# Optimization experiments

Hardware: AMD Instinct MI355X
Metric: run time of the kernel (lower is better)

Reference implementation:

```python
import jax, jax.numpy as jnp
import numpy as np

B, NQ, NKV, D = 2, 2048, 2048, 1024
N_HEADS = 16
D_H = D // N_HEADS


def setup_inputs() -> dict:
    key = jax.random.key(0)
    ks = jax.random.split(key, 10)
    s = 0.02  # weight init scale
    return {
        "q": jax.random.normal(ks[0], (B, NQ, D), jnp.float32),
        "kv": jax.random.normal(ks[1], (B, NKV, D), jnp.float32),
        "Wq": jax.random.normal(ks[2], (D, D), jnp.float32) * s,
        "bq": jnp.zeros((D,), jnp.float32),
        "Wk": jax.random.normal(ks[3], (D, D), jnp.float32) * s,
        "bk": jnp.zeros((D,), jnp.float32),
        "Wv": jax.random.normal(ks[4], (D, D), jnp.float32) * s,
        "bv": jnp.zeros((D,), jnp.float32),
        "Wo": jax.random.normal(ks[5], (D, D), jnp.float32) * s,
        "bo": jnp.zeros((D,), jnp.float32),
    }


def reference(q, kv, Wq, bq, Wk, bk, Wv, bv, Wo, bo):
    # Linear projections (torch Linear: x @ W.T + b)
    qh = q @ Wq.T + bq   # [B, NQ, D]
    kh = kv @ Wk.T + bk  # [B, NKV, D]
    vh = kv @ Wv.T + bv  # [B, NKV, D]
    # Split heads: [B, N, H, d_h]
    qh = qh.reshape(B, NQ, N_HEADS, D_H)
    kh = kh.reshape(B, NKV, N_HEADS, D_H)
    vh = vh.reshape(B, NKV, N_HEADS, D_H)
    scale = 1.0 / jnp.sqrt(jnp.asarray(D_H, qh.dtype))
    # QK^T per head: [B, H, NQ, NKV]
    scores = jnp.einsum("bqhd,bkhd->bhqk", qh, kh) * scale
    att = jax.nn.softmax(scores, axis=-1)
    # dropout p=0.0 -> identity
    out = jnp.einsum("bhqk,bkhd->bqhd", att, vh)  # [B, NQ, H, d_h]
    out = out.reshape(B, NQ, D)
    return out @ Wo.T + bo
```

## Files before the change

kernel.cpp:

```cpp
#include <hip/hip_runtime.h>
#include <cstddef>
#include <cstdint>

using half4v  = __attribute__((ext_vector_type(4))) _Float16;
using half8   = __attribute__((ext_vector_type(8))) _Float16;
using floatx4 = __attribute__((ext_vector_type(4))) float;

#define B_   2
#define NQ_  2048
#define DM   1024
#define NH_  16
#define DH_  64
#define NTILES 32

__device__ __forceinline__ void async16(const _Float16* g, _Float16* l) {
    __builtin_amdgcn_global_load_lds(
        (const __attribute__((address_space(1))) unsigned int*)g,
        (__attribute__((address_space(3))) unsigned int*)l, 16, 0, 0);
}

__global__ __launch_bounds__(256) void cvt_all(
        const float* __restrict__ q,  const float* __restrict__ kv,
        const float* __restrict__ wq, const float* __restrict__ wk,
        const float* __restrict__ wv, const float* __restrict__ wo,
        _Float16* __restrict__ dq,  _Float16* __restrict__ dkv,
        _Float16* __restrict__ dwq, _Float16* __restrict__ dwk,
        _Float16* __restrict__ dwv, _Float16* __restrict__ dwo) {
    int blk = blockIdx.x;
    const float* s;
    _Float16* d;
    int base;
    if (blk < 2048)      { s = q;  d = dq;  base = blk; }
    else if (blk < 4096) { s = kv; d = dkv; base = blk - 2048; }
    else if (blk < 4608) { s = wq; d = dwq; base = blk - 4096; }
    else if (blk < 5120) { s = wk; d = dwk; base = blk - 4608; }
    else if (blk < 5632) { s = wv; d = dwv; base = blk - 5120; }
    else                 { s = wo; d = dwo; base = blk - 5632; }
    int i = base * 256 + threadIdx.x;
    const float4* s4 = (const float4*)s;
    float4 a = s4[2 * i], b = s4[2 * i + 1];
    half8 h;
    h[0] = (_Float16)a.x; h[1] = (_Float16)a.y; h[2] = (_Float16)a.z; h[3] = (_Float16)a.w;
    h[4] = (_Float16)b.x; h[5] = (_Float16)b.y; h[6] = (_Float16)b.z; h[7] = (_Float16)b.w;
    ((half8*)d)[i] = h;
}

__global__ __launch_bounds__(256, 3) void proj_qkv(
        const _Float16* __restrict__ q16, const _Float16* __restrict__ kv16,
        const _Float16* __restrict__ wqp, const _Float16* __restrict__ wkp,
        const _Float16* __restrict__ wvp,
        const float* __restrict__ bqp, const float* __restrict__ bkp,
        const float* __restrict__ bvp,
        _Float16* __restrict__ qh, _Float16* __restrict__ kh,
        _Float16* __restrict__ vt) {
    __shared__ _Float16 As[128 * 64];
    __shared__ _Float16 Bs[128 * 64];

    const int which = blockIdx.x >> 8;
    const int sub = blockIdx.x & 255;
    const _Float16* A = (which == 0) ? q16 : kv16;
    const _Float16* W = (which == 0) ? wqp : (which == 1) ? wkp : wvp;
    const float* bias = (which == 0) ? bqp : (which == 1) ? bkp : bvp;

    const int t = threadIdx.x;
    const int w = t >> 6, lane = t & 63;
    const int r16 = lane & 15, quad = lane >> 4;
    const int bm = (sub & 7) * 4 + ((sub >> 3) & 3);
    const int bn = sub >> 5;
    const int m0 = bm * 128, n0 = bn * 128;
    const int wm = w >> 1, wn = w & 1;

    floatx4 acc[4][4];
#pragma unroll
    for (int i = 0; i < 4; i++)
#pragma unroll
        for (int j = 0; j < 4; j++)
#pragma unroll
            for (int r = 0; r < 4; r++) acc[i][j][r] = 0.f;

    const int ph0 = quad ^ (r16 & 7), ph1 = ph0 ^ 4;

    for (int k0 = 0; k0 < DM; k0 += 64) {
        __syncthreads();
#pragma unroll
        for (int i = 0; i < 4; i++) {
            int P = i * 256 + t;
            int m = P >> 3, c = (P & 7) ^ (m & 7);
            async16(A + (size_t)(m0 + m) * DM + k0 + c * 8, &As[P * 8]);
            async16(W + (size_t)(n0 + m) * DM + k0 + c * 8, &Bs[P * 8]);
        }
        asm volatile("s_waitcnt vmcnt(0)" ::: "memory");
        __syncthreads();

        half8 af[4][2], bf[4][2];
#pragma unroll
        for (int mi = 0; mi < 4; mi++) {
            int m = wm * 64 + mi * 16 + r16;
            af[mi][0] = ((const half8*)As)[m * 8 + ph0];
            af[mi][1] = ((const half8*)As)[m * 8 + ph1];
        }
#pragma unroll
        for (int ni = 0; ni < 4; ni++) {
            int n = wn * 64 + ni * 16 + r16;
            bf[ni][0] = ((const half8*)Bs)[n * 8 + ph0];
            bf[ni][1] = ((const half8*)Bs)[n * 8 + ph1];
        }
#pragma unroll
        for (int kd = 0; kd < 2; kd++)
#pragma unroll
            for (int mi = 0; mi < 4; mi++)
#pragma unroll
                for (int ni = 0; ni < 4; ni++)
                    acc[mi][ni] = __builtin_amdgcn_mfma_f32_16x16x32_f16(
                        af[mi][kd], bf[ni][kd], acc[mi][ni], 0, 0, 0);
    }

    if (which < 2) {
        _Float16* C = (which == 0) ? qh : kh;
        const float esc = (which == 0) ? 0.125f : 1.0f;
#pragma unroll
        for (int mi = 0; mi < 4; mi++)
#pragma unroll
            for (int r = 0; r < 4; r++) {
                int row = m0 + wm * 64 + mi * 16 + quad * 4 + r;
#pragma unroll
                for (int ni = 0; ni < 4; ni++) {
                    int col = n0 + wn * 64 + ni * 16 + r16;
                    C[(size_t)row * DM + col] = (_Float16)((acc[mi][ni][r] + bias[col]) * esc);
                }
            }
    } else {
#pragma unroll
        for (int mi = 0; mi < 4; mi++) {
            int krow = m0 + wm * 64 + mi * 16 + quad * 4;
            int bb = krow >> 11, kk = krow & 2047;
#pragma unroll
            for (int ni = 0; ni < 4; ni++) {
                int col = n0 + wn * 64 + ni * 16 + r16;
                int hh = col >> 6, dd = col & 63;
                float bv = bias[col];
                half4v pk;
#pragma unroll
                for (int r = 0; r < 4; r++) pk[r] = (_Float16)(acc[mi][ni][r] + bv);
                *(half4v*)&vt[((size_t)((bb * NH_ + hh) * DH_ + dd)) * NQ_ + kk] = pk;
            }
        }
    }
}

__global__ __launch_bounds__(256, 4) void attn_mfma(const _Float16* __restrict__ Qg,
                                                    const _Float16* __restrict__ Kg,
                                                    const _Float16* __restrict__ Vt,
                                                    _Float16* __restrict__ Og) {
    __shared__ _Float16 Ps[64 * 64];
    __shared__ _Float16 Ks[2][64 * 64];
    __shared__ _Float16 Vs[2][64 * 64];

    const int t = threadIdx.x, w = t >> 6, lane = t & 63;
    const int r16 = lane & 15, quad = lane >> 4;
    const int blk = blockIdx.x;
    const int bh = (blk & 7) * 4 + ((blk >> 3) & 3);
    const int qt = blk >> 5;
    const int b = bh >> 4, h = bh & 15;

    const _Float16* qbase = Qg + (size_t)(b * NQ_ + qt * 64) * DM + h * DH_;
    const _Float16* kbase = Kg + (size_t)(b * NQ_) * DM + h * DH_;
    const _Float16* vbase = Vt + (size_t)bh * DH_ * NQ_;

#pragma unroll
    for (int i = 0; i < 2; i++) {
        int P = i * 256 + t;
        int m = P >> 3, c = (P & 7) ^ (m & 7);
        async16(qbase + (size_t)m * DM + c * 8, &Ps[P * 8]);
        async16(kbase + (size_t)m * DM + c * 8, &Ks[0][P * 8]);
        async16(vbase + (size_t)m * NQ_ + c * 8, &Vs[0][P * 8]);
    }
    asm volatile("s_waitcnt vmcnt(0)" ::: "memory");
    __syncthreads();

    const int ph0 = quad ^ (r16 & 7), ph1 = ph0 ^ 4;
    half8 Qf[2];
    {
        int m = w * 16 + r16;
        Qf[0] = ((const half8*)Ps)[m * 8 + ph0];
        Qf[1] = ((const half8*)Ps)[m * 8 + ph1];
    }

    floatx4 oaccT[4];
    float lacc = 0.f;
#pragma unroll
    for (int nd = 0; nd < 4; nd++)
#pragma unroll
        for (int r = 0; r < 4; r++) oaccT[nd][r] = 0.f;

    for (int kt = 0; kt < NTILES; kt++) {
        const int cur = kt & 1;
        asm volatile("s_waitcnt vmcnt(0)" ::: "memory");
        __syncthreads();

        if (kt + 1 < NTILES) {
            const int nxt = cur ^ 1;
#pragma unroll
            for (int i = 0; i < 2; i++) {
                int P = i * 256 + t;
                int m = P >> 3, c = (P & 7) ^ (m & 7);
                async16(kbase + (size_t)((kt + 1) * 64 + m) * DM + c * 8, &Ks[nxt][P * 8]);
                async16(vbase + (size_t)m * NQ_ + (kt + 1) * 64 + c * 8, &Vs[nxt][P * 8]);
            }
        }

        floatx4 sacc[4];
#pragma unroll
        for (int nk = 0; nk < 4; nk++)
#pragma unroll
            for (int r = 0; r < 4; r++) sacc[nk][r] = 0.f;
#pragma unroll
        for (int kd = 0; kd < 2; kd++)
#pragma unroll
            for (int nk = 0; nk < 4; nk++) {
                half8 kf = ((const half8*)Ks[cur])[(nk * 16 + r16) * 8 + (kd ? ph1 : ph0)];
                sacc[nk] = __builtin_amdgcn_mfma_f32_16x16x32_f16(kf, Qf[kd], sacc[nk], 0, 0, 0);
            }

        const int q = w * 16 + r16;
#pragma unroll
        for (int nk = 0; nk < 4; nk++) {
            float p0 = __expf(sacc[nk][0]);
            float p1 = __expf(sacc[nk][1]);
            float p2 = __expf(sacc[nk][2]);
            float p3 = __expf(sacc[nk][3]);
            lacc += (p0 + p1) + (p2 + p3);
            half4v pk;
            pk[0] = (_Float16)p0; pk[1] = (_Float16)p1;
            pk[2] = (_Float16)p2; pk[3] = (_Float16)p3;
            int phys = (nk * 2 + (quad >> 1)) ^ (r16 & 7);
            *(half4v*)&Ps[q * 64 + phys * 8 + (quad & 1) * 4] = pk;
        }

#pragma unroll
        for (int ks = 0; ks < 2; ks++) {
            half8 pf = ((const half8*)Ps)[q * 8 + ((ks * 4 + quad) ^ (r16 & 7))];
#pragma unroll
            for (int nd = 0; nd < 4; nd++) {
                half8 vf = ((const half8*)Vs[cur])[(nd * 16 + r16) * 8 + ((ks * 4 + quad) ^ (r16 & 7))];
                oaccT[nd] = __builtin_amdgcn_mfma_f32_16x16x32_f16(vf, pf, oaccT[nd], 0, 0, 0);
            }
        }
    }

    {
        float l = lacc;
        l += __shfl_xor(l, 16);
        l += __shfl_xor(l, 32);
        float inv = 1.f / l;
        int qrow = b * NQ_ + qt * 64 + w * 16 + r16;
#pragma unroll
        for (int nd = 0; nd < 4; nd++) {
            half4v o;
#pragma unroll
            for (int r = 0; r < 4; r++) o[r] = (_Float16)(oaccT[nd][r] * inv);
            *(half4v*)&Og[(size_t)qrow * DM + h * DH_ + nd * 16 + quad * 4] = o;
        }
    }
}

__global__ __launch_bounds__(256, 4) void gemm_o(const _Float16* __restrict__ A,
                                                 const _Float16* __restrict__ W,
                                                 const float* __restrict__ bias,
                                                 float* __restrict__ C) {
    __shared__ _Float16 As[64 * 64];
    __shared__ _Float16 Bs[64 * 64];

    const int t = threadIdx.x;
    const int w = t >> 6, lane = t & 63;
    const int r16 = lane & 15, quad = lane >> 4;
    const int blk = blockIdx.x;
    const int bm = (blk & 7) * 8 + ((blk >> 3) & 7);
    const int bn = blk >> 6;
    const int m0 = bm * 64, n0 = bn * 64;
    const int wm = w >> 1, wn = w & 1;

    floatx4 acc[2][2];
#pragma unroll
    for (int i = 0; i < 2; i++)
#pragma unroll
        for (int j = 0; j < 2; j++)
#pragma unroll
            for (int r = 0; r < 4; r++) acc[i][j][r] = 0.f;

    const int ph0 = quad ^ (r16 & 7), ph1 = ph0 ^ 4;

    for (int k0 = 0; k0 < DM; k0 += 64) {
        __syncthreads();
#pragma unroll
        for (int i = 0; i < 2; i++) {
            int P = i * 256 + t;
            int m = P >> 3, c = (P & 7) ^ (m & 7);
            async16(A + (size_t)(m0 + m) * DM + k0 + c * 8, &As[P * 8]);
            async16(W + (size_t)(n0 + m) * DM + k0 + c * 8, &Bs[P * 8]);
        }
        asm volatile("s_waitcnt vmcnt(0)" ::: "memory");
        __syncthreads();

        half8 af[2][2], bf[2][2];
#pragma unroll
        for (int mi = 0; mi < 2; mi++) {
            int m = wm * 32 + mi * 16 + r16;
            af[mi][0] = ((const half8*)As)[m * 8 + ph0];
            af[mi][1] = ((const half8*)As)[m * 8 + ph1];
        }
#pragma unroll
        for (int ni = 0; ni < 2; ni++) {
            int n = wn * 32 + ni * 16 + r16;
            bf[ni][0] = ((const half8*)Bs)[n * 8 + ph0];
            bf[ni][1] = ((const half8*)Bs)[n * 8 + ph1];
        }
#pragma unroll
        for (int kd = 0; kd < 2; kd++)
#pragma unroll
            for (int mi = 0; mi < 2; mi++)
#pragma unroll
                for (int ni = 0; ni < 2; ni++)
                    acc[mi][ni] = __builtin_amdgcn_mfma_f32_16x16x32_f16(
                        af[mi][kd], bf[ni][kd], acc[mi][ni], 0, 0, 0);
    }

#pragma unroll
    for (int mi = 0; mi < 2; mi++)
#pragma unroll
        for (int r = 0; r < 4; r++) {
            int row = m0 + wm * 32 + mi * 16 + quad * 4 + r;
#pragma unroll
            for (int ni = 0; ni < 2; ni++) {
                int col = n0 + wn * 32 + ni * 16 + r16;
                C[(size_t)row * DM + col] = acc[mi][ni][r] + bias[col];
            }
        }
}

extern "C" void kernel_launch(void* const* d_in, const int* in_sizes, int n_in,
                              void* d_out, int out_size, void* d_ws, size_t ws_size,
                              hipStream_t stream) {
    const float* q  = (const float*)d_in[0];
    const float* kv = (const float*)d_in[1];
    const float* Wq = (const float*)d_in[2];
    const float* bq = (const float*)d_in[3];
    const float* Wk = (const float*)d_in[4];
    const float* bk = (const float*)d_in[5];
    const float* Wv = (const float*)d_in[6];
    const float* bv = (const float*)d_in[7];
    const float* Wo = (const float*)d_in[8];
    const float* bo = (const float*)d_in[9];

    char* ws = (char*)d_ws;
    _Float16* q16  = (_Float16*)(ws);
    _Float16* kv16 = (_Float16*)(ws + (size_t)(8  << 20));
    _Float16* w16q = (_Float16*)(ws + (size_t)(16 << 20));
    _Float16* w16k = (_Float16*)(ws + (size_t)(18 << 20));
    _Float16* w16v = (_Float16*)(ws + (size_t)(20 << 20));
    _Float16* w16o = (_Float16*)(ws + (size_t)(22 << 20));
    _Float16* qh16 = (_Float16*)(ws + (size_t)(24 << 20));
    _Float16* kh16 = (_Float16*)(ws + (size_t)(32 << 20));
    _Float16* vt16 = (_Float16*)(ws + (size_t)(40 << 20));
    _Float16* ao16 = (_Float16*)(ws + (size_t)(48 << 20));

    cvt_all<<<6144, 256, 0, stream>>>(q, kv, Wq, Wk, Wv, Wo,
                                      q16, kv16, w16q, w16k, w16v, w16o);

    proj_qkv<<<768, 256, 0, stream>>>(q16, kv16, w16q, w16k, w16v,
                                      bq, bk, bv, qh16, kh16, vt16);

    attn_mfma<<<1024, 256, 0, stream>>>(qh16, kh16, vt16, ao16);

    gemm_o<<<1024, 256, 0, stream>>>(ao16, w16o, bo, (float*)d_out);
}
```

Measured before the change: 200.5 us.

## Split attention warps 2x2 over query and key halves with LDS reduction

Each warp in the attention kernel now owns 32 query rows and half of each 64-key tile, instead of 16 query rows and the full key tile. Each loaded K and V fragment is reused across two query sub-tiles, which roughly halves the LDS fragment reads per MFMA. The P staging buffer becomes per-warp, which removes cross-warp coupling in Ps. The cost is doubled accumulator registers, plus an epilogue that reduces the two key-half partial outputs and row sums through shared memory, with extra barriers.

```diff
diff --git a/kernel.cpp b/kernel.cpp
--- a/kernel.cpp
+++ b/kernel.cpp
@@ -158,6 +158,7 @@
 
     const int t = threadIdx.x, w = t >> 6, lane = t & 63;
     const int r16 = lane & 15, quad = lane >> 4;
+    const int wq = w >> 1, wk = w & 1;
     const int blk = blockIdx.x;
     const int bh = (blk & 7) * 4 + ((blk >> 3) & 3);
     const int qt = blk >> 5;
@@ -179,19 +180,24 @@
     __syncthreads();
 
     const int ph0 = quad ^ (r16 & 7), ph1 = ph0 ^ 4;
-    half8 Qf[2];
-    {
-        int m = w * 16 + r16;
-        Qf[0] = ((const half8*)Ps)[m * 8 + ph0];
-        Qf[1] = ((const half8*)Ps)[m * 8 + ph1];
-    }
-
-    floatx4 oaccT[4];
-    float lacc = 0.f;
+    half8 Qf[2][2];
+#pragma unroll
+    for (int nq = 0; nq < 2; nq++) {
+        int m = wq * 32 + nq * 16 + r16;
+        Qf[nq][0] = ((const half8*)Ps)[m * 8 + ph0];
+        Qf[nq][1] = ((const half8*)Ps)[m * 8 + ph1];
+    }
+
+    floatx4 oaccT[4][2];
+    float lacc[2] = {0.f, 0.f};
 #pragma unroll
     for (int nd = 0; nd < 4; nd++)
 #pragma unroll
-        for (int r = 0; r < 4; r++) oaccT[nd][r] = 0.f;
+        for (int nq = 0; nq < 2; nq++)
+#pragma unroll
+            for (int r = 0; r < 4; r++) oaccT[nd][nq][r] = 0.f;
+
+    _Float16* preg = &Ps[w * 1024];
 
     for (int kt = 0; kt < NTILES; kt++) {
         const int cur = kt & 1;
@@ -209,57 +215,88 @@
             }
         }
 
-        floatx4 sacc[4];
-#pragma unroll
-        for (int nk = 0; nk < 4; nk++)
-#pragma unroll
-            for (int r = 0; r < 4; r++) sacc[nk][r] = 0.f;
+        floatx4 sacc[2][2];
+#pragma unroll
+        for (int nk = 0; nk < 2; nk++)
+#pragma unroll
+            for (int nq = 0; nq < 2; nq++)
+#pragma unroll
+                for (int r = 0; r < 4; r++) sacc[nk][nq][r] = 0.f;
 #pragma unroll
         for (int kd = 0; kd < 2; kd++)
 #pragma unroll
-            for (int nk = 0; nk < 4; nk++) {
-                half8 kf = ((const half8*)Ks[cur])[(nk * 16 + r16) * 8 + (kd ? ph1 : ph0)];
-                sacc[nk] = __builtin_amdgcn_mfma_f32_16x16x32_f16(kf, Qf[kd], sacc[nk], 0, 0, 0);
-            }
-
-        const int q = w * 16 + r16;
-#pragma unroll
-        for (int nk = 0; nk < 4; nk++) {
-            float p0 = __expf(sacc[nk][0]);
-            float p1 = __expf(sacc[nk][1]);
-            float p2 = __expf(sacc[nk][2]);
-            float p3 = __expf(sacc[nk][3]);
-            lacc += (p0 + p1) + (p2 + p3);
-            half4v pk;
-            pk[0] = (_Float16)p0; pk[1] = (_Float16)p1;
-            pk[2] = (_Float16)p2; pk[3] = (_Float16)p3;
-            int phys = (nk * 2 + (quad >> 1)) ^ (r16 & 7);
-            *(half4v*)&Ps[q * 64 + phys * 8 + (quad & 1) * 4] = pk;
-        }
-
-#pragma unroll
-        for (int ks = 0; ks < 2; ks++) {
-            half8 pf = ((const half8*)Ps)[q * 8 + ((ks * 4 + quad) ^ (r16 & 7))];
+            for (int nk = 0; nk < 2; nk++) {
+                half8 kf = ((const half8*)Ks[cur])[(wk * 32 + nk * 16 + r16) * 8 + (kd ? ph1 : ph0)];
+#pragma unroll
+                for (int nq = 0; nq < 2; nq++)
+                    sacc[nk][nq] = __builtin_amdgcn_mfma_f32_16x16x32_f16(
+                        kf, Qf[nq][kd], sacc[nk][nq], 0, 0, 0);
+            }
+
+#pragma unroll
+        for (int nk = 0; nk < 2; nk++)
+#pragma unroll
+            for (int nq = 0; nq < 2; nq++) {
+                float p0 = __expf(sacc[nk][nq][0]);
+                float p1 = __expf(sacc[nk][nq][1]);
+                float p2 = __expf(sacc[nk][nq][2]);
+                float p3 = __expf(sacc[nk][nq][3]);
+                lacc[nq] += (p0 + p1) + (p2 + p3);
+                half4v pk;
+                pk[0] = (_Float16)p0; pk[1] = (_Float16)p1;
+                pk[2] = (_Float16)p2; pk[3] = (_Float16)p3;
+                int ql = nq * 16 + r16;
+                int c16 = (nk * 2 + (quad >> 1)) ^ (ql & 3);
+                *(half4v*)&preg[ql * 32 + c16 * 8 + (quad & 1) * 4] = pk;
+            }
+
+        half8 pf[2];
+#pragma unroll
+        for (int nq = 0; nq < 2; nq++)
+            pf[nq] = ((const half8*)preg)[(nq * 16 + r16) * 4 + (quad ^ (r16 & 3))];
+#pragma unroll
+        for (int nd = 0; nd < 4; nd++) {
+            half8 vf = ((const half8*)Vs[cur])[(nd * 16 + r16) * 8 + ((wk * 4 + quad) ^ (r16 & 7))];
+#pragma unroll
+            for (int nq = 0; nq < 2; nq++)
+                oaccT[nd][nq] = __builtin_amdgcn_mfma_f32_16x16x32_f16(
+                    vf, pf[nq], oaccT[nd][nq], 0, 0, 0);
+        }
+    }
+
+#pragma unroll
+    for (int nq = 0; nq < 2; nq++) {
+        lacc[nq] += __shfl_xor(lacc[nq], 16);
+        lacc[nq] += __shfl_xor(lacc[nq], 32);
+    }
+    __syncthreads();
+    float* ob = (wq == 0) ? (float*)Ks : (float*)Vs;
+    float* Lbuf = (float*)Ps;
+    if (wk == 1) {
+#pragma unroll
+        for (int nd = 0; nd < 4; nd++)
+#pragma unroll
+            for (int nq = 0; nq < 2; nq++)
+                *(floatx4*)&ob[(nq * 16 + r16) * 68 + nd * 16 + quad * 4] = oaccT[nd][nq];
+#pragma unroll
+        for (int nq = 0; nq < 2; nq++)
+            Lbuf[wq * 32 + nq * 16 + r16] = lacc[nq];
+    }
+    __syncthreads();
+    if (wk == 0) {
+#pragma unroll
+        for (int nq = 0; nq < 2; nq++) {
+            float inv = 1.f / (lacc[nq] + Lbuf[wq * 32 + nq * 16 + r16]);
+            int qrow = b * NQ_ + qt * 64 + wq * 32 + nq * 16 + r16;
 #pragma unroll
             for (int nd = 0; nd < 4; nd++) {
-                half8 vf = ((const half8*)Vs[cur])[(nd * 16 + r16) * 8 + ((ks * 4 + quad) ^ (r16 & 7))];
-                oaccT[nd] = __builtin_amdgcn_mfma_f32_16x16x32_f16(vf, pf, oaccT[nd], 0, 0, 0);
-            }
-        }
-    }
-
-    {
-        float l = lacc;
-        l += __shfl_xor(l, 16);
-        l += __shfl_xor(l, 32);
-        float inv = 1.f / l;
-        int qrow = b * NQ_ + qt * 64 + w * 16 + r16;
-#pragma unroll
-        for (int nd = 0; nd < 4; nd++) {
-            half4v o;
-#pragma unroll
-            for (int r = 0; r < 4; r++) o[r] = (_Float16)(oaccT[nd][r] * inv);
-            *(half4v*)&Og[(size_t)qrow * DM + h * DH_ + nd * 16 + quad * 4] = o;
+                floatx4 part = *(floatx4*)&ob[(nq * 16 + r16) * 68 + nd * 16 + quad * 4];
+                half4v o;
+#pragma unroll
+                for (int r = 0; r < 4; r++)
+                    o[r] = (_Float16)((oaccT[nd][nq][r] + part[r]) * inv);
+                *(half4v*)&Og[(size_t)qrow * DM + h * DH_ + nd * 16 + quad * 4] = o;
+            }
         }
     }
 }
```

Result: slower. 207.4 us (+3.5%).

## Restructure attention kernel to 32x32 MFMA with KV-split warps and register P

Applied to the files above, without the earlier changes.

The attention kernel now runs 512 threads per block, arranged as 2 query-warp rows by 4 key-split warps. It uses 32x32x16 MFMA and processes 128-key tiles, so there are half as many iterations. The probability tile stays in registers, rearranged with lane shuffles instead of a round trip through LDS. Partial output accumulators from the key-split warps are reduced through LDS at the end. This trades double buffering for single-buffered K/V with two barriers per iteration, plus extra reduction work in the epilogue.

```diff
diff --git a/kernel.cpp b/kernel.cpp
--- a/kernel.cpp
+++ b/kernel.cpp
@@ -2,21 +2,29 @@
 #include <cstddef>
 #include <cstdint>
 
-using half4v  = __attribute__((ext_vector_type(4))) _Float16;
-using half8   = __attribute__((ext_vector_type(8))) _Float16;
-using floatx4 = __attribute__((ext_vector_type(4))) float;
+using half4v   = __attribute__((ext_vector_type(4))) _Float16;
+using half8    = __attribute__((ext_vector_type(8))) _Float16;
+using floatx4  = __attribute__((ext_vector_type(4))) float;
+using floatx16 = __attribute__((ext_vector_type(16))) float;
+using uintx4   = __attribute__((ext_vector_type(4))) unsigned;
 
 #define B_   2
 #define NQ_  2048
 #define DM   1024
 #define NH_  16
 #define DH_  64
-#define NTILES 32
+#define KITERS 16
 
 __device__ __forceinline__ void async16(const _Float16* g, _Float16* l) {
     __builtin_amdgcn_global_load_lds(
         (const __attribute__((address_space(1))) unsigned int*)g,
         (__attribute__((address_space(3))) unsigned int*)l, 16, 0, 0);
+}
+
+__device__ __forceinline__ unsigned pkh(float a, float b) {
+    union { _Float16 h[2]; unsigned u; } x;
+    x.h[0] = (_Float16)a; x.h[1] = (_Float16)b;
+    return x.u;
 }
 
 __global__ __launch_bounds__(256) void cvt_all(
@@ -148,16 +156,17 @@
     }
 }
 
-__global__ __launch_bounds__(256, 4) void attn_mfma(const _Float16* __restrict__ Qg,
+__global__ __launch_bounds__(512, 8) void attn_mfma(const _Float16* __restrict__ Qg,
                                                     const _Float16* __restrict__ Kg,
                                                     const _Float16* __restrict__ Vt,
                                                     _Float16* __restrict__ Og) {
-    __shared__ _Float16 Ps[64 * 64];
-    __shared__ _Float16 Ks[2][64 * 64];
-    __shared__ _Float16 Vs[2][64 * 64];
+    __shared__ _Float16 Ks[128 * 64];
+    __shared__ _Float16 Vs[64 * 128];
+    __shared__ _Float16 Qs[64 * 64];
 
     const int t = threadIdx.x, w = t >> 6, lane = t & 63;
-    const int r16 = lane & 15, quad = lane >> 4;
+    const int l31 = lane & 31, hi = lane >> 5;
+    const int wq = w >> 2, wk = w & 3;
     const int blk = blockIdx.x;
     const int bh = (blk & 7) * 4 + ((blk >> 3) & 3);
     const int qt = blk >> 5;
@@ -167,100 +176,184 @@
     const _Float16* kbase = Kg + (size_t)(b * NQ_) * DM + h * DH_;
     const _Float16* vbase = Vt + (size_t)bh * DH_ * NQ_;
 
-#pragma unroll
-    for (int i = 0; i < 2; i++) {
-        int P = i * 256 + t;
-        int m = P >> 3, c = (P & 7) ^ (m & 7);
-        async16(qbase + (size_t)m * DM + c * 8, &Ps[P * 8]);
-        async16(kbase + (size_t)m * DM + c * 8, &Ks[0][P * 8]);
-        async16(vbase + (size_t)m * NQ_ + c * 8, &Vs[0][P * 8]);
+    {
+        int m = t >> 3, c = (t & 7) ^ (m & 7);
+        async16(qbase + (size_t)m * DM + c * 8, &Qs[t * 8]);
+#pragma unroll
+        for (int r = 0; r < 2; r++) {
+            int P = r * 512 + t;
+            int km = P >> 3, kc = (P & 7) ^ (km & 7);
+            async16(kbase + (size_t)km * DM + kc * 8, &Ks[P * 8]);
+        }
     }
     asm volatile("s_waitcnt vmcnt(0)" ::: "memory");
     __syncthreads();
 
-    const int ph0 = quad ^ (r16 & 7), ph1 = ph0 ^ 4;
-    half8 Qf[2];
+    floatx16 oacc0, oacc1;
+#pragma unroll
+    for (int r = 0; r < 16; r++) { oacc0[r] = 0.f; oacc1[r] = 0.f; }
+    float lacc = 0.f;
+
+    const int qrow = wq * 32 + l31;
+    const int krow = wk * 32 + l31;
+
+    for (int i = 0; i < KITERS; i++) {
+#pragma unroll
+        for (int r = 0; r < 2; r++) {
+            int P = r * 512 + t;
+            int vm = P >> 4, vc = (P & 15) ^ (vm & 15);
+            async16(vbase + (size_t)vm * NQ_ + i * 128 + vc * 8, &Vs[P * 8]);
+        }
+
+        floatx16 sacc;
+#pragma unroll
+        for (int r = 0; r < 16; r++) sacc[r] = 0.f;
+#pragma unroll
+        for (int step = 0; step < 4; step++) {
+            half8 kf = ((const half8*)Ks)[krow * 8 + ((step * 2 + hi) ^ (l31 & 7))];
+            half8 qf = ((const half8*)Qs)[qrow * 8 + ((step * 2 + hi) ^ (l31 & 7))];
+            sacc = __builtin_amdgcn_mfma_f32_32x32x16_f16(kf, qf, sacc, 0, 0, 0);
+        }
+
+#pragma unroll
+        for (int r = 0; r < 16; r++) sacc[r] = __expf(sacc[r]);
+#pragma unroll
+        for (int r = 0; r < 16; r++) lacc += sacc[r];
+
+        half8 pf0, pf1;
+        {
+            unsigned a0 = pkh(sacc[0], sacc[1]),  a1 = pkh(sacc[2], sacc[3]);
+            unsigned b0 = pkh(sacc[4], sacc[5]),  b1 = pkh(sacc[6], sacc[7]);
+            unsigned s0 = hi ? a0 : b0, s1 = hi ? a1 : b1;
+            unsigned r0 = (unsigned)__shfl_xor((int)s0, 32);
+            unsigned r1 = (unsigned)__shfl_xor((int)s1, 32);
+            union { unsigned u[4]; half8 h; } pu;
+            pu.u[0] = hi ? r0 : a0; pu.u[1] = hi ? r1 : a1;
+            pu.u[2] = hi ? b0 : r0; pu.u[3] = hi ? b1 : r1;
+            pf0 = pu.h;
+        }
+        {
+            unsigned a0 = pkh(sacc[8], sacc[9]),   a1 = pkh(sacc[10], sacc[11]);
+            unsigned b0 = pkh(sacc[12], sacc[13]), b1 = pkh(sacc[14], sacc[15]);
+            unsigned s0 = hi ? a0 : b0, s1 = hi ? a1 : b1;
+            unsigned r0 = (unsigned)__shfl_xor((int)s0, 32);
+            unsigned r1 = (unsigned)__shfl_xor((int)s1, 32);
+            union { unsigned u[4]; half8 h; } pu;
+            pu.u[0] = hi ? r0 : a0; pu.u[1] = hi ? r1 : a1;
+            pu.u[2] = hi ? b0 : r0; pu.u[3] = hi ? b1 : r1;
+            pf1 = pu.h;
+        }
+
+        asm volatile("s_waitcnt vmcnt(0)" ::: "memory");
+        __syncthreads();
+
+        if (i + 1 < KITERS) {
+#pragma unroll
+            for (int r = 0; r < 2; r++) {
+                int P = r * 512 + t;
+                int km = P >> 3, kc = (P & 7) ^ (km & 7);
+                async16(kbase + (size_t)((i + 1) * 128 + km) * DM + kc * 8, &Ks[P * 8]);
+            }
+        }
+
+#pragma unroll
+        for (int kstep = 0; kstep < 2; kstep++) {
+            half8 pfk = kstep ? pf1 : pf0;
+            {
+                half8 vf = ((const half8*)Vs)[(0 * 32 + l31) * 16 + ((wk * 4 + kstep * 2 + hi) ^ (l31 & 15))];
+                oacc0 = __builtin_amdgcn_mfma_f32_32x32x16_f16(vf, pfk, oacc0, 0, 0, 0);
+            }
+            {
+                half8 vf = ((const half8*)Vs)[(1 * 32 + l31) * 16 + ((wk * 4 + kstep * 2 + hi) ^ (l31 & 15))];
+                oacc1 = __builtin_amdgcn_mfma_f32_32x32x16_f16(vf, pfk, oacc1, 0, 0, 0);
+            }
+        }
+
+        asm volatile("s_waitcnt vmcnt(0)" ::: "memory");
+        __syncthreads();
+    }
+
+    float* Ksf = (float*)Ks;
+    float* Vsf = (float*)Vs;
+    float* Lb  = (float*)Qs;
+    float* RA = Ksf + wq * 2048;
+    float* RB = Vsf + wq * 2048;
+
+    float lfull = lacc + __shfl_xor(lacc, 32);
+
+    if (lane < 32) Lb[wk * 64 + wq * 32 + l31] = lfull;
+    if (wk == 1) {
+#pragma unroll
+        for (int r = 0; r < 16; r++) {
+            int d0 = (r & 3) + 8 * ((r >> 2) & 3) + 4 * hi;
+            RA[l31 * 64 + (d0 ^ l31)] = oacc0[r];
+            RA[l31 * 64 + ((d0 + 32) ^ l31)] = oacc1[r];
+        }
+    }
+    if (wk == 3) {
+#pragma unroll
+        for (int r = 0; r < 16; r++) {
+            int d0 = (r & 3) + 8 * ((r >> 2) & 3) + 4 * hi;
+            RB[l31 * 64 + (d0 ^ l31)] = oacc0[r];
+            RB[l31 * 64 + ((d0 + 32) ^ l31)] = oacc1[r];
+        }
+    }
+    __syncthreads();
+
+    float linv = 0.f;
+    if (wk == 0) {
+        int idx = wq * 32 + l31;
+        linv = 1.f / (Lb[idx] + Lb[64 + idx] + Lb[128 + idx] + Lb[192 + idx]);
+#pragma unroll
+        for (int r = 0; r < 16; r++) {
+            int d0 = (r & 3) + 8 * ((r >> 2) & 3) + 4 * hi;
+            oacc0[r] += RA[l31 * 64 + (d0 ^ l31)];
+            oacc1[r] += RA[l31 * 64 + ((d0 + 32) ^ l31)];
+        }
+    }
+    if (wk == 2) {
+#pragma unroll
+        for (int r = 0; r < 16; r++) {
+            int d0 = (r & 3) + 8 * ((r >> 2) & 3) + 4 * hi;
+            oacc0[r] += RB[l31 * 64 + (d0 ^ l31)];
+            oacc1[r] += RB[l31 * 64 + ((d0 + 32) ^ l31)];
+        }
+    }
+    __syncthreads();
+
+    if (wk == 2) {
+#pragma unroll
+        for (int r = 0; r < 16; r++) {
+            int d0 = (r & 3) + 8 * ((r >> 2) & 3) + 4 * hi;
+            RA[l31 * 64 + (d0 ^ l31)] = oacc0[r];
+            RA[l31 * 64 + ((d0 + 32) ^ l31)] = oacc1[r];
+        }
+    }
+    __syncthreads();
+
+    if (wk == 0) {
+#pragma unroll
+        for (int r = 0; r < 16; r++) {
+            int d0 = (r & 3) + 8 * ((r >> 2) & 3) + 4 * hi;
+            float v0 = (oacc0[r] + RA[l31 * 64 + (d0 ^ l31)]) * linv;
+            float v1 = (oacc1[r] + RA[l31 * 64 + ((d0 + 32) ^ l31)]) * linv;
+            RA[l31 * 64 + (d0 ^ l31)] = v0;
+            RA[l31 * 64 + ((d0 + 32) ^ l31)] = v1;
+        }
+    }
+    __syncthreads();
+
     {
-        int m = w * 16 + r16;
-        Qf[0] = ((const half8*)Ps)[m * 8 + ph0];
-        Qf[1] = ((const half8*)Ps)[m * 8 + ph1];
-    }
-
-    floatx4 oaccT[4];
-    float lacc = 0.f;
-#pragma unroll
-    for (int nd = 0; nd < 4; nd++)
-#pragma unroll
-        for (int r = 0; r < 4; r++) oaccT[nd][r] = 0.f;
-
-    for (int kt = 0; kt < NTILES; kt++) {
-        const int cur = kt & 1;
-        asm volatile("s_waitcnt vmcnt(0)" ::: "memory");
-        __syncthreads();
-
-        if (kt + 1 < NTILES) {
-            const int nxt = cur ^ 1;
-#pragma unroll
-            for (int i = 0; i < 2; i++) {
-                int P = i * 256 + t;
-                int m = P >> 3, c = (P & 7) ^ (m & 7);
-                async16(kbase + (size_t)((kt + 1) * 64 + m) * DM + c * 8, &Ks[nxt][P * 8]);
-                async16(vbase + (size_t)m * NQ_ + (kt + 1) * 64 + c * 8, &Vs[nxt][P * 8]);
-            }
-        }
-
-        floatx4 sacc[4];
-#pragma unroll
-        for (int nk = 0; nk < 4; nk++)
-#pragma unroll
-            for (int r = 0; r < 4; r++) sacc[nk][r] = 0.f;
-#pragma unroll
-        for (int kd = 0; kd < 2; kd++)
-#pragma unroll
-            for (int nk = 0; nk < 4; nk++) {
-                half8 kf = ((const half8*)Ks[cur])[(nk * 16 + r16) * 8 + (kd ? ph1 : ph0)];
-                sacc[nk] = __builtin_amdgcn_mfma_f32_16x16x32_f16(kf, Qf[kd], sacc[nk], 0, 0, 0);
-            }
-
-        const int q = w * 16 + r16;
-#pragma unroll
-        for (int nk = 0; nk < 4; nk++) {
-            float p0 = __expf(sacc[nk][0]);
-            float p1 = __expf(sacc[nk][1]);
-            float p2 = __expf(sacc[nk][2]);
-            float p3 = __expf(sacc[nk][3]);
-            lacc += (p0 + p1) + (p2 + p3);
-            half4v pk;
-            pk[0] = (_Float16)p0; pk[1] = (_Float16)p1;
-            pk[2] = (_Float16)p2; pk[3] = (_Float16)p3;
-            int phys = (nk * 2 + (quad >> 1)) ^ (r16 & 7);
-            *(half4v*)&Ps[q * 64 + phys * 8 + (quad & 1) * 4] = pk;
-        }
-
-#pragma unroll
-        for (int ks = 0; ks < 2; ks++) {
-            half8 pf = ((const half8*)Ps)[q * 8 + ((ks * 4 + quad) ^ (r16 & 7))];
-#pragma unroll
-            for (int nd = 0; nd < 4; nd++) {
-                half8 vf = ((const half8*)Vs[cur])[(nd * 16 + r16) * 8 + ((ks * 4 + quad) ^ (r16 & 7))];
-                oaccT[nd] = __builtin_amdgcn_mfma_f32_16x16x32_f16(vf, pf, oaccT[nd], 0, 0, 0);
-            }
-        }
-    }
-
-    {
-        float l = lacc;
-        l += __shfl_xor(l, 16);
-        l += __shfl_xor(l, 32);
-        float inv = 1.f / l;
-        int qrow = b * NQ_ + qt * 64 + w * 16 + r16;
-#pragma unroll
-        for (int nd = 0; nd < 4; nd++) {
-            half4v o;
-#pragma unroll
-            for (int r = 0; r < 4; r++) o[r] = (_Float16)(oaccT[nd][r] * inv);
-            *(half4v*)&Og[(size_t)qrow * DM + h * DH_ + nd * 16 + quad * 4] = o;
-        }
+        int qq = t >> 3, cc = t & 7;
+        const float* R = Ksf + (qq >> 5) * 2048;
+        int ql = qq & 31;
+        half8 o;
+#pragma unroll
+        for (int j = 0; j < 8; j++) {
+            int d = cc * 8 + j;
+            o[j] = (_Float16)R[ql * 64 + (d ^ ql)];
+        }
+        *(half8*)&Og[(size_t)(b * NQ_ + qt * 64 + qq) * DM + h * DH_ + cc * 8] = o;
     }
 }
 
@@ -370,7 +463,7 @@
     proj_qkv<<<768, 256, 0, stream>>>(q16, kv16, w16q, w16k, w16v,
                                       bq, bk, bv, qh16, kh16, vt16);
 
-    attn_mfma<<<1024, 256, 0, stream>>>(qh16, kh16, vt16, ao16);
+    attn_mfma<<<1024, 512, 0, stream>>>(qh16, kh16, vt16, ao16);
 
     gemm_o<<<1024, 256, 0, stream>>>(ao16, w16o, bo, (float*)d_out);
 }
```

Result: slower. 396.4 us (+97.7%).

## Split attention key tile across wave pairs with LDS reduction of partial outputs

Applied to the files above, without the earlier changes.

Doubles the attention block to 8 waves, with each pair of waves sharing a 16-row query slice and splitting the 64-key tile into two 32-key halves. Each wave computes half the scores and half the PV product, and the two partial output accumulators and row sums are combined through LDS at the end. The intent is more waves in flight to hide LDS and global latency, and less MFMA work per wave per tile. The cost is an extra reduction step and extra barriers. Each wave also issues fewer MFMAs per barrier, so synchronisation overhead is larger relative to compute.

```diff
diff --git a/kernel.cpp b/kernel.cpp
--- a/kernel.cpp
+++ b/kernel.cpp
@@ -148,7 +148,7 @@
     }
 }
 
-__global__ __launch_bounds__(256, 4) void attn_mfma(const _Float16* __restrict__ Qg,
+__global__ __launch_bounds__(512, 6) void attn_mfma(const _Float16* __restrict__ Qg,
                                                     const _Float16* __restrict__ Kg,
                                                     const _Float16* __restrict__ Vt,
                                                     _Float16* __restrict__ Og) {
@@ -158,6 +158,7 @@
 
     const int t = threadIdx.x, w = t >> 6, lane = t & 63;
     const int r16 = lane & 15, quad = lane >> 4;
+    const int wq = w >> 1, wk = w & 1;
     const int blk = blockIdx.x;
     const int bh = (blk & 7) * 4 + ((blk >> 3) & 3);
     const int qt = blk >> 5;
@@ -167,24 +168,21 @@
     const _Float16* kbase = Kg + (size_t)(b * NQ_) * DM + h * DH_;
     const _Float16* vbase = Vt + (size_t)bh * DH_ * NQ_;
 
-#pragma unroll
-    for (int i = 0; i < 2; i++) {
-        int P = i * 256 + t;
-        int m = P >> 3, c = (P & 7) ^ (m & 7);
-        async16(qbase + (size_t)m * DM + c * 8, &Ps[P * 8]);
-        async16(kbase + (size_t)m * DM + c * 8, &Ks[0][P * 8]);
-        async16(vbase + (size_t)m * NQ_ + c * 8, &Vs[0][P * 8]);
+    {
+        int m = t >> 3, c = (t & 7) ^ (m & 7);
+        async16(qbase + (size_t)m * DM + c * 8, &Ps[t * 8]);
+        async16(kbase + (size_t)m * DM + c * 8, &Ks[0][t * 8]);
+        async16(vbase + (size_t)m * NQ_ + c * 8, &Vs[0][t * 8]);
     }
     asm volatile("s_waitcnt vmcnt(0)" ::: "memory");
     __syncthreads();
 
     const int ph0 = quad ^ (r16 & 7), ph1 = ph0 ^ 4;
+    const int q = wq * 16 + r16;
     half8 Qf[2];
-    {
-        int m = w * 16 + r16;
-        Qf[0] = ((const half8*)Ps)[m * 8 + ph0];
-        Qf[1] = ((const half8*)Ps)[m * 8 + ph1];
-    }
+    Qf[0] = ((const half8*)Ps)[q * 8 + ph0];
+    Qf[1] = ((const half8*)Ps)[q * 8 + ph1];
+    __syncthreads();
 
     floatx4 oaccT[4];
     float lacc = 0.f;
@@ -200,65 +198,78 @@
 
         if (kt + 1 < NTILES) {
             const int nxt = cur ^ 1;
-#pragma unroll
-            for (int i = 0; i < 2; i++) {
-                int P = i * 256 + t;
-                int m = P >> 3, c = (P & 7) ^ (m & 7);
-                async16(kbase + (size_t)((kt + 1) * 64 + m) * DM + c * 8, &Ks[nxt][P * 8]);
-                async16(vbase + (size_t)m * NQ_ + (kt + 1) * 64 + c * 8, &Vs[nxt][P * 8]);
-            }
-        }
-
-        floatx4 sacc[4];
-#pragma unroll
-        for (int nk = 0; nk < 4; nk++)
-#pragma unroll
-            for (int r = 0; r < 4; r++) sacc[nk][r] = 0.f;
+            int m = t >> 3, c = (t & 7) ^ (m & 7);
+            async16(kbase + (size_t)((kt + 1) * 64 + m) * DM + c * 8, &Ks[nxt][t * 8]);
+            async16(vbase + (size_t)m * NQ_ + (kt + 1) * 64 + c * 8, &Vs[nxt][t * 8]);
+        }
+
+        floatx4 sacc[2];
+#pragma unroll
+        for (int nk2 = 0; nk2 < 2; nk2++)
+#pragma unroll
+            for (int r = 0; r < 4; r++) sacc[nk2][r] = 0.f;
 #pragma unroll
         for (int kd = 0; kd < 2; kd++)
 #pragma unroll
-            for (int nk = 0; nk < 4; nk++) {
-                half8 kf = ((const half8*)Ks[cur])[(nk * 16 + r16) * 8 + (kd ? ph1 : ph0)];
-                sacc[nk] = __builtin_amdgcn_mfma_f32_16x16x32_f16(kf, Qf[kd], sacc[nk], 0, 0, 0);
-            }
-
-        const int q = w * 16 + r16;
-#pragma unroll
-        for (int nk = 0; nk < 4; nk++) {
-            float p0 = __expf(sacc[nk][0]);
-            float p1 = __expf(sacc[nk][1]);
-            float p2 = __expf(sacc[nk][2]);
-            float p3 = __expf(sacc[nk][3]);
+            for (int nk2 = 0; nk2 < 2; nk2++) {
+                half8 kf = ((const half8*)Ks[cur])[(wk * 32 + nk2 * 16 + r16) * 8 + (kd ? ph1 : ph0)];
+                sacc[nk2] = __builtin_amdgcn_mfma_f32_16x16x32_f16(kf, Qf[kd], sacc[nk2], 0, 0, 0);
+            }
+
+#pragma unroll
+        for (int nk2 = 0; nk2 < 2; nk2++) {
+            float p0 = __expf(sacc[nk2][0]);
+            float p1 = __expf(sacc[nk2][1]);
+            float p2 = __expf(sacc[nk2][2]);
+            float p3 = __expf(sacc[nk2][3]);
             lacc += (p0 + p1) + (p2 + p3);
             half4v pk;
             pk[0] = (_Float16)p0; pk[1] = (_Float16)p1;
             pk[2] = (_Float16)p2; pk[3] = (_Float16)p3;
-            int phys = (nk * 2 + (quad >> 1)) ^ (r16 & 7);
-            *(half4v*)&Ps[q * 64 + phys * 8 + (quad & 1) * 4] = pk;
-        }
-
-#pragma unroll
-        for (int ks = 0; ks < 2; ks++) {
-            half8 pf = ((const half8*)Ps)[q * 8 + ((ks * 4 + quad) ^ (r16 & 7))];
-#pragma unroll
-            for (int nd = 0; nd < 4; nd++) {
-                half8 vf = ((const half8*)Vs[cur])[(nd * 16 + r16) * 8 + ((ks * 4 + quad) ^ (r16 & 7))];
-                oaccT[nd] = __builtin_amdgcn_mfma_f32_16x16x32_f16(vf, pf, oaccT[nd], 0, 0, 0);
-            }
-        }
-    }
-
-    {
-        float l = lacc;
-        l += __shfl_xor(l, 16);
-        l += __shfl_xor(l, 32);
-        float inv = 1.f / l;
-        int qrow = b * NQ_ + qt * 64 + w * 16 + r16;
+            int chunk = wk * 4 + nk2 * 2 + (quad >> 1);
+            *(half4v*)&Ps[q * 64 + (chunk ^ (r16 & 7)) * 8 + (quad & 1) * 4] = pk;
+        }
+
+        half8 pf = ((const half8*)Ps)[q * 8 + ((wk * 4 + quad) ^ (r16 & 7))];
+#pragma unroll
+        for (int nd = 0; nd < 4; nd++) {
+            half8 vf = ((const half8*)Vs[cur])[(nd * 16 + r16) * 8 + ((wk * 4 + quad) ^ (r16 & 7))];
+            oaccT[nd] = __builtin_amdgcn_mfma_f32_16x16x32_f16(vf, pf, oaccT[nd], 0, 0, 0);
+        }
+    }
+
+    lacc += __shfl_xor(lacc, 16);
+    lacc += __shfl_xor(lacc, 32);
+    __syncthreads();
+
+    float* Rg = (float*)Ks;
+    float* Lb = (float*)Ps;
+    if (quad == 0) Lb[wk * 64 + q] = lacc;
+    if (wk == 1) {
+        float* R = Rg + wq * 1024;
+#pragma unroll
+        for (int nd = 0; nd < 4; nd++)
+#pragma unroll
+            for (int r = 0; r < 4; r++) {
+                int d = nd * 16 + quad * 4 + r;
+                R[r16 * 64 + (d ^ (r16 << 2))] = oaccT[nd][r];
+            }
+    }
+    __syncthreads();
+
+    if (wk == 0) {
+        float linv = 1.f / (Lb[q] + Lb[64 + q]);
+        const float* R = Rg + wq * 1024;
+        int qrow = b * NQ_ + qt * 64 + q;
 #pragma unroll
         for (int nd = 0; nd < 4; nd++) {
             half4v o;
 #pragma unroll
-            for (int r = 0; r < 4; r++) o[r] = (_Float16)(oaccT[nd][r] * inv);
+            for (int r = 0; r < 4; r++) {
+                int d = nd * 16 + quad * 4 + r;
+                float v = oaccT[nd][r] + R[r16 * 64 + (d ^ (r16 << 2))];
+                o[r] = (_Float16)(v * linv);
+            }
             *(half4v*)&Og[(size_t)qrow * DM + h * DH_ + nd * 16 + quad * 4] = o;
         }
     }
@@ -370,7 +381,7 @@
     proj_qkv<<<768, 256, 0, stream>>>(q16, kv16, w16q, w16k, w16v,
                                       bq, bk, bv, qh16, kh16, vt16);
 
-    attn_mfma<<<1024, 256, 0, stream>>>(qh16, kh16, vt16, ao16);
+    attn_mfma<<<1024, 512, 0, stream>>>(qh16, kh16, vt16, ao16);
 
     gemm_o<<<1024, 256, 0, stream>>>(ao16, w16o, bo, (float*)d_out);
 }
```

Measured after the change: 203.9 us. Within noise of the previous version (+1.7%).
